# Kernel tuning notes

Hardware: AMD Instinct MI355X
Metric: run time of the kernel (lower is better)

## Reference

```python
import jax, jax.numpy as jnp
import numpy as np


def setup_inputs() -> dict:
    key = jax.random.key(0)
    k1, k2 = jax.random.split(key)
    pred = jax.random.normal(k1, (8, 4096, 2), dtype=jnp.float32)
    target = jax.random.normal(k2, (8, 4096, 2), dtype=jnp.float32)
    return {"pred": pred, "target": target}


def reference(pred, target):
    # pred: [B, N, D], target: [B, M, D]
    # pairwise euclidean distances per batch: [B, N, M]
    diff = pred[:, :, None, :] - target[:, None, :, :]  # [B, N, M, D]
    dist = jnp.sqrt(jnp.sum(diff * diff, axis=-1))       # [B, N, M]
    # directed Hausdorff h(a,b) = max_i min_j d(a_i, b_j)
    h_ab = jnp.max(jnp.min(dist, axis=2), axis=1)        # [B]
    h_ba = jnp.max(jnp.min(dist, axis=1), axis=1)        # [B]
    score = jnp.maximum(h_ab, h_ba)                      # symmetric Hausdorff per batch
    return jnp.mean(score)
```

## Files before the change

kernel.cpp:

```cpp
#include <hip/hip_runtime.h>
#include <math.h>


#define B 8
#define N 4096
#define TPB 256
#define JC 8
#define JTILE (N / JC)
#define NT (JTILE / 32)
#define IBLK 128
#define NIB (N / IBLK)
#define ITILES (N / TPB)

typedef _Float16 half8 __attribute__((ext_vector_type(8)));
typedef float f32x16 __attribute__((ext_vector_type(16)));

__global__ __launch_bounds__(TPB) void hk_partial(const float* __restrict__ pred,
                                                  const float* __restrict__ target,
                                                  float* __restrict__ pw) {
    const int ibk = blockIdx.x & (NIB - 1);
    const int jc  = blockIdx.x >> 5;
    const int b   = blockIdx.y;
    const int dir = blockIdx.z;

    const float2* __restrict__ P =
        reinterpret_cast<const float2*>(dir == 0 ? pred : target) + (size_t)b * N;
    const float2* __restrict__ Q =
        reinterpret_cast<const float2*>(dir == 0 ? target : pred) + (size_t)b * N
        + (size_t)jc * JTILE;

    __shared__ half8 sA[NT * 64];

    for (int s = threadIdx.x; s < JTILE; s += TPB) {
        float2 q = Q[s];
        _Float16 xh = (_Float16)q.x;
        _Float16 xl = (_Float16)(q.x - (float)xh);
        _Float16 yh = (_Float16)q.y;
        _Float16 yl = (_Float16)(q.y - (float)yh);
        float qq = fmaf(q.x, q.x, q.y * q.y);
        _Float16 qqh = (_Float16)qq;
        _Float16 qql = (_Float16)(qq - (float)qqh);
        _Float16 nxh = (_Float16)(-2.f * (float)xh);
        _Float16 nxl = (_Float16)(-2.f * (float)xl);
        _Float16 nyh = (_Float16)(-2.f * (float)yh);
        _Float16 nyl = (_Float16)(-2.f * (float)yl);
        const _Float16 z = (_Float16)0.f;
        int t = s >> 5, m = s & 31;
        sA[t * 64 + m]      = (half8){nxh, nxh, nxl, nxl, nyh, nyh, nyl, nyl};
        sA[t * 64 + 32 + m] = (half8){qqh, qql, z, z, z, z, z, z};
    }

    const int lane = threadIdx.x & 63;
    const int wave = threadIdx.x >> 6;
    const int col  = lane & 31;
    const int i    = ibk * IBLK + wave * 32 + col;

    half8 bf;
    float pp = 0.f;
    if (lane < 32) {
        float2 p = P[i];
        _Float16 xh = (_Float16)p.x;
        _Float16 xl = (_Float16)(p.x - (float)xh);
        _Float16 yh = (_Float16)p.y;
        _Float16 yl = (_Float16)(p.y - (float)yh);
        bf = (half8){xh, xl, xh, xl, yh, yl, yh, yl};
        pp = fmaf(p.x, p.x, p.y * p.y);
    } else {
        const _Float16 one = (_Float16)1.f;
        const _Float16 z   = (_Float16)0.f;
        bf = (half8){one, one, z, z, z, z, z, z};
    }

    __syncthreads();

    float rm[8];
    #pragma unroll
    for (int r = 0; r < 8; ++r) rm[r] = 3.402823466e38f;

    #pragma unroll 2
    for (int t = 0; t < NT; ++t) {
        half8 a = sA[t * 64 + lane];
        f32x16 acc = {};
        acc = __builtin_amdgcn_mfma_f32_32x32x16_f16(a, bf, acc, 0, 0, 0);
        #pragma unroll
        for (int r = 0; r < 8; ++r)
            rm[r] = fminf(rm[r], fminf(acc[2 * r], acc[2 * r + 1]));
    }

    float mn = fminf(fminf(fminf(rm[0], rm[1]), fminf(rm[2], rm[3])),
                     fminf(fminf(rm[4], rm[5]), fminf(rm[6], rm[7])));
    mn = fminf(mn, __shfl_xor(mn, 32, 64));

    if (lane < 32) {
        float* dst = pw + (size_t)((dir * B + b) * JC + jc) * N;
        dst[i] = mn + pp;
    }
}

__global__ __launch_bounds__(TPB) void hk_maxred(const float* __restrict__ pw,
                                                 float* __restrict__ pw2) {
    const int tile = blockIdx.x;
    const int b    = blockIdx.y;
    const int dir  = blockIdx.z;
    const int t    = threadIdx.x;

    const float* base = pw + (size_t)((dir * B + b) * JC) * N + tile * TPB + t;
    float mnv = base[0];
    #pragma unroll
    for (int jc = 1; jc < JC; ++jc) mnv = fminf(mnv, base[(size_t)jc * N]);

    float mx = mnv;
    #pragma unroll
    for (int off = 32; off > 0; off >>= 1)
        mx = fmaxf(mx, __shfl_down(mx, off, 64));

    __shared__ float sred[TPB / 64];
    if ((t & 63) == 0) sred[t >> 6] = mx;
    __syncthreads();
    if (t == 0) {
        float bm = sred[0];
        #pragma unroll
        for (int w = 1; w < TPB / 64; ++w) bm = fmaxf(bm, sred[w]);
        pw2[(dir * B + b) * ITILES + tile] = bm;
    }
}

__global__ __launch_bounds__(64) void hk_final(const float* __restrict__ pw2,
                                               float* __restrict__ out) {
    const int t = threadIdx.x;
    __shared__ float h2[2 * B];
    if (t < 2 * B) {
        float mx = pw2[t * ITILES];
        #pragma unroll
        for (int k = 1; k < ITILES; ++k) mx = fmaxf(mx, pw2[t * ITILES + k]);
        h2[t] = mx;
    }
    __syncthreads();
    if (t == 0) {
        float s = 0.f;
        #pragma unroll
        for (int b = 0; b < B; ++b)
            s += sqrtf(fmaxf(fmaxf(h2[b], h2[B + b]), 0.f));
        out[0] = s * (1.0f / B);
    }
}

extern "C" void kernel_launch(void* const* d_in, const int* in_sizes, int n_in,
                              void* d_out, int out_size, void* d_ws, size_t ws_size,
                              hipStream_t stream) {
    const float* pred   = (const float*)d_in[0];
    const float* target = (const float*)d_in[1];
    float* out = (float*)d_out;
    float* pw  = (float*)d_ws;
    float* pw2 = (float*)((char*)d_ws + (size_t)2 * B * JC * N * sizeof(float));

    dim3 g1(NIB * JC, B, 2);
    hk_partial<<<g1, TPB, 0, stream>>>(pred, target, pw);
    dim3 g2(ITILES, B, 2);
    hk_maxred<<<g2, TPB, 0, stream>>>(pw, pw2);
    hk_final<<<1, 64, 0, stream>>>(pw2, out);
}
```

Before: 79.28 us.

## Fuse j-split reduction into partial kernel by looping over all targets per block

Each block now walks the full target set in 1024-point shared-memory chunks instead of splitting j across 8 blocks. The per-row min and the per-block max are done in-kernel, so the intermediate kernel and its large workspace traffic go away. This removes one launch and the write and read of the 2*B*JC*N partial array. The cost is 8x fewer blocks (512), each running a longer serial loop with extra barriers, which lowers parallelism on a GPU with many CUs.

After: 83.25 us. 1.05x slower.

```diff
diff --git a/kernel.cpp b/kernel.cpp
--- a/kernel.cpp
+++ b/kernel.cpp
@@ -5,12 +5,11 @@
 #define B 8
 #define N 4096
 #define TPB 256
-#define JC 8
-#define JTILE (N / JC)
-#define NT (JTILE / 32)
 #define IBLK 128
 #define NIB (N / IBLK)
-#define ITILES (N / TPB)
+#define JCHUNK 1024
+#define NCHUNK (N / JCHUNK)
+#define NTC (JCHUNK / 32)
 
 typedef _Float16 half8 __attribute__((ext_vector_type(8)));
 typedef float f32x16 __attribute__((ext_vector_type(16)));
@@ -18,37 +17,17 @@
 __global__ __launch_bounds__(TPB) void hk_partial(const float* __restrict__ pred,
                                                   const float* __restrict__ target,
                                                   float* __restrict__ pw) {
-    const int ibk = blockIdx.x & (NIB - 1);
-    const int jc  = blockIdx.x >> 5;
+    const int ibk = blockIdx.x;
     const int b   = blockIdx.y;
     const int dir = blockIdx.z;
 
     const float2* __restrict__ P =
         reinterpret_cast<const float2*>(dir == 0 ? pred : target) + (size_t)b * N;
     const float2* __restrict__ Q =
-        reinterpret_cast<const float2*>(dir == 0 ? target : pred) + (size_t)b * N
-        + (size_t)jc * JTILE;
+        reinterpret_cast<const float2*>(dir == 0 ? target : pred) + (size_t)b * N;
 
-    __shared__ half8 sA[NT * 64];
-
-    for (int s = threadIdx.x; s < JTILE; s += TPB) {
-        float2 q = Q[s];
-        _Float16 xh = (_Float16)q.x;
-        _Float16 xl = (_Float16)(q.x - (float)xh);
-        _Float16 yh = (_Float16)q.y;
-        _Float16 yl = (_Float16)(q.y - (float)yh);
-        float qq = fmaf(q.x, q.x, q.y * q.y);
-        _Float16 qqh = (_Float16)qq;
-        _Float16 qql = (_Float16)(qq - (float)qqh);
-        _Float16 nxh = (_Float16)(-2.f * (float)xh);
-        _Float16 nxl = (_Float16)(-2.f * (float)xl);
-        _Float16 nyh = (_Float16)(-2.f * (float)yh);
-        _Float16 nyl = (_Float16)(-2.f * (float)yl);
-        const _Float16 z = (_Float16)0.f;
-        int t = s >> 5, m = s & 31;
-        sA[t * 64 + m]      = (half8){nxh, nxh, nxl, nxl, nyh, nyh, nyl, nyl};
-        sA[t * 64 + 32 + m] = (half8){qqh, qql, z, z, z, z, z, z};
-    }
+    __shared__ half8 sA[NTC * 64];
+    __shared__ float sred[TPB / 64];
 
     const int lane = threadIdx.x & 63;
     const int wave = threadIdx.x >> 6;
@@ -71,68 +50,69 @@
         bf = (half8){one, one, z, z, z, z, z, z};
     }
 
-    __syncthreads();
-
+    const f32x16 zacc = {};
     float rm[8];
     #pragma unroll
     for (int r = 0; r < 8; ++r) rm[r] = 3.402823466e38f;
 
-    #pragma unroll 2
-    for (int t = 0; t < NT; ++t) {
-        half8 a = sA[t * 64 + lane];
-        f32x16 acc = {};
-        acc = __builtin_amdgcn_mfma_f32_32x32x16_f16(a, bf, acc, 0, 0, 0);
-        #pragma unroll
-        for (int r = 0; r < 8; ++r)
-            rm[r] = fminf(rm[r], fminf(acc[2 * r], acc[2 * r + 1]));
+    for (int c = 0; c < NCHUNK; ++c) {
+        for (int s = threadIdx.x; s < JCHUNK; s += TPB) {
+            float2 q = Q[c * JCHUNK + s];
+            _Float16 xh = (_Float16)q.x;
+            _Float16 xl = (_Float16)(q.x - (float)xh);
+            _Float16 yh = (_Float16)q.y;
+            _Float16 yl = (_Float16)(q.y - (float)yh);
+            float qq = fmaf(q.x, q.x, q.y * q.y);
+            _Float16 qqh = (_Float16)qq;
+            _Float16 qql = (_Float16)(qq - (float)qqh);
+            _Float16 nxh = (_Float16)(-2.f * (float)xh);
+            _Float16 nxl = (_Float16)(-2.f * (float)xl);
+            _Float16 nyh = (_Float16)(-2.f * (float)yh);
+            _Float16 nyl = (_Float16)(-2.f * (float)yl);
+            const _Float16 z = (_Float16)0.f;
+            int t = s >> 5, m = s & 31;
+            sA[t * 64 + m]      = (half8){nxh, nxh, nxl, nxl, nyh, nyh, nyl, nyl};
+            sA[t * 64 + 32 + m] = (half8){qqh, qql, z, z, z, z, z, z};
+        }
+        __syncthreads();
+
+        #pragma unroll 4
+        for (int t = 0; t < NTC; ++t) {
+            half8 a = sA[t * 64 + lane];
+            f32x16 d = __builtin_amdgcn_mfma_f32_32x32x16_f16(a, bf, zacc, 0, 0, 0);
+            #pragma unroll
+            for (int r = 0; r < 8; ++r)
+                rm[r] = fminf(rm[r], fminf(d[2 * r], d[2 * r + 1]));
+        }
+        __syncthreads();
     }
 
     float mn = fminf(fminf(fminf(rm[0], rm[1]), fminf(rm[2], rm[3])),
                      fminf(fminf(rm[4], rm[5]), fminf(rm[6], rm[7])));
     mn = fminf(mn, __shfl_xor(mn, 32, 64));
 
-    if (lane < 32) {
-        float* dst = pw + (size_t)((dir * B + b) * JC + jc) * N;
-        dst[i] = mn + pp;
+    float val = (lane < 32) ? mn + pp : -3.402823466e38f;
+    #pragma unroll
+    for (int off = 16; off > 0; off >>= 1)
+        val = fmaxf(val, __shfl_xor(val, off, 64));
+    if (lane == 0) sred[wave] = val;
+    __syncthreads();
+    if (threadIdx.x == 0) {
+        float m = sred[0];
+        #pragma unroll
+        for (int w = 1; w < TPB / 64; ++w) m = fmaxf(m, sred[w]);
+        pw[(dir * B + b) * NIB + ibk] = m;
     }
 }
 
-__global__ __launch_bounds__(TPB) void hk_maxred(const float* __restrict__ pw,
-                                                 float* __restrict__ pw2) {
-    const int tile = blockIdx.x;
-    const int b    = blockIdx.y;
-    const int dir  = blockIdx.z;
-    const int t    = threadIdx.x;
-
-    const float* base = pw + (size_t)((dir * B + b) * JC) * N + tile * TPB + t;
-    float mnv = base[0];
-    #pragma unroll
-    for (int jc = 1; jc < JC; ++jc) mnv = fminf(mnv, base[(size_t)jc * N]);
-
-    float mx = mnv;
-    #pragma unroll
-    for (int off = 32; off > 0; off >>= 1)
-        mx = fmaxf(mx, __shfl_down(mx, off, 64));
-
-    __shared__ float sred[TPB / 64];
-    if ((t & 63) == 0) sred[t >> 6] = mx;
-    __syncthreads();
-    if (t == 0) {
-        float bm = sred[0];
-        #pragma unroll
-        for (int w = 1; w < TPB / 64; ++w) bm = fmaxf(bm, sred[w]);
-        pw2[(dir * B + b) * ITILES + tile] = bm;
-    }
-}
-
-__global__ __launch_bounds__(64) void hk_final(const float* __restrict__ pw2,
+__global__ __launch_bounds__(64) void hk_final(const float* __restrict__ pw,
                                                float* __restrict__ out) {
     const int t = threadIdx.x;
     __shared__ float h2[2 * B];
     if (t < 2 * B) {
-        float mx = pw2[t * ITILES];
+        float mx = pw[t * NIB];
         #pragma unroll
-        for (int k = 1; k < ITILES; ++k) mx = fmaxf(mx, pw2[t * ITILES + k]);
+        for (int k = 1; k < NIB; ++k) mx = fmaxf(mx, pw[t * NIB + k]);
         h2[t] = mx;
     }
     __syncthreads();
@@ -152,11 +132,8 @@
     const float* target = (const float*)d_in[1];
     float* out = (float*)d_out;
     float* pw  = (float*)d_ws;
-    float* pw2 = (float*)((char*)d_ws + (size_t)2 * B * JC * N * sizeof(float));
 
-    dim3 g1(NIB * JC, B, 2);
+    dim3 g1(NIB, B, 2);
     hk_partial<<<g1, TPB, 0, stream>>>(pred, target, pw);
-    dim3 g2(ITILES, B, 2);
-    hk_maxred<<<g2, TPB, 0, stream>>>(pw, pw2);
-    hk_final<<<1, 64, 0, stream>>>(pw2, out);
+    hk_final<<<1, 64, 0, stream>>>(pw, out);
 }
```
